# Performance work log

Measured on AMD Instinct MI355X. Metric: run time of the kernel, lower is better.

The kernel has to match this reference:

```python
import jax, jax.numpy as jnp
import numpy as np

MAXU = 6          # init arg maxU
MAXV = 6          # init arg maxV (ratio=None)
TRUNC = 4         # cfg.TRUNCATED_SIZE; cfg.TRUNCATED=True, cfg.FLOW_REG_BY_MAX=True


def setup_inputs() -> dict:
    key = jax.random.key(0)
    B, H, W = 8, 128, 160
    U, V = 2 * MAXU + 1, 2 * MAXV + 1
    x = jax.random.normal(key, (B, 1, U, V, H, W), dtype=jnp.float32)
    return {"x": x}


def reference(x):
    # x: [B,1,U,V,H,W] cost volume
    x = x[:, 0]                                   # [B,U,V,H,W]
    b, u, v, h, w = x.shape

    # --- truncation mask (cfg.TRUNCATED) ---
    # argmax over flattened (u,v); scatter one-hot + MaxPool3d((2t+1,2t+1,1))
    # is equivalent to a +-t box around the per-pixel argmax location.
    idx = jnp.argmax(x.reshape(b, u * v, h, w), axis=1)   # [B,H,W] int
    ui = (idx // v)[:, None, None]                        # [B,1,1,H,W]
    vi = (idx % v)[:, None, None]
    ugrid = jnp.arange(u).reshape(1, u, 1, 1, 1)
    vgrid = jnp.arange(v).reshape(1, 1, v, 1, 1)
    mask = (jnp.abs(ugrid - ui) <= TRUNC) & (jnp.abs(vgrid - vi) <= TRUNC)
    xm = jnp.where(mask, x, -jnp.inf)

    # --- softmax over the U*V displacement hypotheses (FLOW_REG_BY_MAX) ---
    p = jax.nn.softmax(xm.reshape(b, u * v, h, w), axis=1).reshape(b, u, v, h, w)

    dispU = jnp.arange(-MAXU, MAXU + 1, dtype=x.dtype)    # [U]
    dispV = jnp.arange(-MAXV, MAXV + 1, dtype=x.dtype)    # [V]
    flowU = jnp.einsum('buvhw,u->bhw', p, dispU)
    flowV = jnp.einsum('buvhw,v->bhw', p, dispV)
    return jnp.stack((flowU, flowV), axis=1)              # [B,2,H,W]
```

## Files before the change

### kernel.cpp

```cpp
#include <hip/hip_runtime.h>
#include <math.h>

#define Udim 13
#define Vdim 13
#define Hdim 128
#define Wdim 160
#define HW (Hdim * Wdim)
#define UV (Udim * Vdim)
#define TRUNC 4
#define NPIX (8 * HW)
#define NPL 85

__global__ __launch_bounds__(256, 3) void flow_regression_kernel(
    const float* __restrict__ x, float* __restrict__ out) {
    int t    = threadIdx.x;
    int lane = t & 63;
    int g    = lane >> 5;
    int p32  = lane & 31;
    int wave = t >> 6;
    int pixel = blockIdx.x * 128 + wave * 32 + p32;
    int b  = pixel / HW;
    int hw = pixel - b * HW;

    const float* base = x + (size_t)b * UV * HW + hw + (size_t)(g * NPL) * HW;

    float vals[NPL];
    #pragma unroll
    for (int i = 0; i < NPL - 1; ++i) vals[i] = base[(size_t)i * HW];
    vals[NPL - 1] = (g == 0) ? base[(size_t)(NPL - 1) * HW] : -INFINITY;

    float m = vals[0];
    int mi = 0;
    #pragma unroll
    for (int i = 1; i < NPL; ++i)
        if (vals[i] > m) { m = vals[i]; mi = i; }
    mi += g * NPL;

    float om = __shfl_xor(m, 32);
    int   oi = __shfl_xor(mi, 32);
    if (om > m || (om == m && oi < mi)) { m = om; mi = oi; }

    int ui = (mi * 158) >> 11;
    int vi = mi - ui * Vdim;

    float s = 0.f, su = 0.f, sv = 0.f;
    int u = g ? 6 : 0, v = g ? 7 : 0;
    #pragma unroll
    for (int i = 0; i < NPL; ++i) {
        bool in = (u - ui <= TRUNC) && (ui - u <= TRUNC) &&
                  (v - vi <= TRUNC) && (vi - v <= TRUNC);
        float e = in ? __expf(vals[i] - m) : 0.f;
        s  += e;
        su += e * (float)(u - 6);
        sv += e * (float)(v - 6);
        if (++v == Vdim) { v = 0; ++u; }
    }
    s  += __shfl_xor(s, 32);
    su += __shfl_xor(su, 32);
    sv += __shfl_xor(sv, 32);

    if (g == 0) {
        float inv = 1.0f / s;
        float* ob = out + (size_t)b * 2 * HW + hw;
        ob[0]  = su * inv;
        ob[HW] = sv * inv;
    }
}

extern "C" void kernel_launch(void* const* d_in, const int* in_sizes, int n_in,
                              void* d_out, int out_size, void* d_ws, size_t ws_size,
                              hipStream_t stream) {
    const float* x = (const float*)d_in[0];
    float* out = (float*)d_out;
    flow_regression_kernel<<<NPIX / 128, 256, 0, stream>>>(x, out);
}
```

Before: 162.8 us.

## Stage cost volume through LDS with direct global-to-LDS loads, split planes four ways

Each block now stages all 169 planes for 64 pixels into shared memory using global_load_lds, then four lane groups each scan about 43 planes for the argmax and the masked softmax sums. The partial results are combined with shuffles. The goal is to cut per-thread register pressure from the 85-value array and raise occupancy, while keeping loads coalesced. In exchange it uses about 43KB of LDS per block, which limits how many blocks fit per CU, adds a full barrier before any compute, and replaces the constant-multiply divide with a real one.

```diff
diff --git a/kernel.cpp b/kernel.cpp
--- a/kernel.cpp
+++ b/kernel.cpp
@@ -3,65 +3,82 @@
 
 #define Udim 13
 #define Vdim 13
-#define Hdim 128
-#define Wdim 160
-#define HW (Hdim * Wdim)
-#define UV (Udim * Vdim)
+#define HW 20480
+#define UV 169
 #define TRUNC 4
 #define NPIX (8 * HW)
-#define NPL 85
+#define PIX_PER_BLK 64
+#define LDS_STRIDE 65
 
-__global__ __launch_bounds__(256, 3) void flow_regression_kernel(
+typedef const __attribute__((address_space(1))) void glb_void;
+typedef __attribute__((address_space(3))) void lds_void;
+
+__global__ __launch_bounds__(256) void flow_regression_kernel(
     const float* __restrict__ x, float* __restrict__ out) {
+    __shared__ float lds[UV * LDS_STRIDE];
+
     int t    = threadIdx.x;
+    int wave = t >> 6;
     int lane = t & 63;
-    int g    = lane >> 5;
-    int p32  = lane & 31;
-    int wave = t >> 6;
-    int pixel = blockIdx.x * 128 + wave * 32 + p32;
-    int b  = pixel / HW;
-    int hw = pixel - b * HW;
+    int pix0 = blockIdx.x * PIX_PER_BLK;
+    int b    = pix0 / HW;
+    int hw0  = pix0 - b * HW;
 
-    const float* base = x + (size_t)b * UV * HW + hw + (size_t)(g * NPL) * HW;
+    const float* gbase = x + (size_t)b * UV * HW + hw0;
 
-    float vals[NPL];
+    for (int pl = wave; pl < UV; pl += 4) {
+        const float* gp = gbase + (size_t)pl * HW + lane;
+        float* lp = &lds[pl * LDS_STRIDE];
+        __builtin_amdgcn_global_load_lds((glb_void*)gp, (lds_void*)lp, 4, 0, 0);
+    }
+    __builtin_amdgcn_s_waitcnt(0);
+    __syncthreads();
+
+    int q    = lane >> 4;
+    int pcol = (wave << 4) | (lane & 15);
+    int base_pl = q * 43;
+    int npl     = (q == 3) ? 40 : 43;
+
+    float m = -INFINITY;
+    int mi = base_pl;
     #pragma unroll
-    for (int i = 0; i < NPL - 1; ++i) vals[i] = base[(size_t)i * HW];
-    vals[NPL - 1] = (g == 0) ? base[(size_t)(NPL - 1) * HW] : -INFINITY;
-
-    float m = vals[0];
-    int mi = 0;
-    #pragma unroll
-    for (int i = 1; i < NPL; ++i)
-        if (vals[i] > m) { m = vals[i]; mi = i; }
-    mi += g * NPL;
-
-    float om = __shfl_xor(m, 32);
-    int   oi = __shfl_xor(mi, 32);
-    if (om > m || (om == m && oi < mi)) { m = om; mi = oi; }
-
-    int ui = (mi * 158) >> 11;
+    for (int i = 0; i < 43; ++i) {
+        if (i < npl) {
+            float v = lds[(base_pl + i) * LDS_STRIDE + pcol];
+            if (v > m) { m = v; mi = base_pl + i; }
+        }
+    }
+    {
+        float om = __shfl_xor(m, 16); int oi = __shfl_xor(mi, 16);
+        if (om > m || (om == m && oi < mi)) { m = om; mi = oi; }
+        om = __shfl_xor(m, 32); oi = __shfl_xor(mi, 32);
+        if (om > m || (om == m && oi < mi)) { m = om; mi = oi; }
+    }
+    int ui = mi / Vdim;
     int vi = mi - ui * Vdim;
 
     float s = 0.f, su = 0.f, sv = 0.f;
-    int u = g ? 6 : 0, v = g ? 7 : 0;
+    int u = base_pl / Vdim;
+    int v = base_pl - u * Vdim;
     #pragma unroll
-    for (int i = 0; i < NPL; ++i) {
-        bool in = (u - ui <= TRUNC) && (ui - u <= TRUNC) &&
-                  (v - vi <= TRUNC) && (vi - v <= TRUNC);
-        float e = in ? __expf(vals[i] - m) : 0.f;
-        s  += e;
-        su += e * (float)(u - 6);
-        sv += e * (float)(v - 6);
+    for (int i = 0; i < 43; ++i) {
+        if (i < npl) {
+            float val = lds[(base_pl + i) * LDS_STRIDE + pcol];
+            bool in = (u - ui <= TRUNC) && (ui - u <= TRUNC) &&
+                      (v - vi <= TRUNC) && (vi - v <= TRUNC);
+            float e = in ? __expf(val - m) : 0.f;
+            s  += e;
+            su += e * (float)(u - 6);
+            sv += e * (float)(v - 6);
+        }
         if (++v == Vdim) { v = 0; ++u; }
     }
-    s  += __shfl_xor(s, 32);
-    su += __shfl_xor(su, 32);
-    sv += __shfl_xor(sv, 32);
+    s  += __shfl_xor(s, 16);  su += __shfl_xor(su, 16);  sv += __shfl_xor(sv, 16);
+    s  += __shfl_xor(s, 32);  su += __shfl_xor(su, 32);  sv += __shfl_xor(sv, 32);
 
-    if (g == 0) {
+    if (q == 0) {
         float inv = 1.0f / s;
-        float* ob = out + (size_t)b * 2 * HW + hw;
+        float* ob = out + (size_t)b * 2 * HW + (hw0 + pcol);
         ob[0]  = su * inv;
         ob[HW] = sv * inv;
     }
@@ -72,5 +89,5 @@
                               hipStream_t stream) {
     const float* x = (const float*)d_in[0];
     float* out = (float*)d_out;
-    flow_regression_kernel<<<NPIX / 128, 256, 0, stream>>>(x, out);
+    flow_regression_kernel<<<NPIX / PIX_PER_BLK, 256, 0, stream>>>(x, out);
 }
```

New measurement: 163.1 us. Within noise of the previous version (+0.2%).

## Split each pixel's displacement planes across four lane groups instead of two

Applied to the files above, without the earlier changes.

Each pixel's 169 cost planes are now spread over four 16-lane groups of 43 planes each, instead of two 32-lane groups of 85. This cuts per-thread register arrays and raises occupancy (launch bounds 3→4), giving more loads in flight for this bandwidth-bound kernel. The cost is an extra shuffle stage for both the argmax and sum reductions. Each wave also reads only 16 contiguous pixels per plane, which gives shorter coalesced segments, and the grid doubles.

```diff
diff --git a/kernel.cpp b/kernel.cpp
--- a/kernel.cpp
+++ b/kernel.cpp
@@ -1,50 +1,58 @@
 #include <hip/hip_runtime.h>
 #include <math.h>
 
-#define Udim 13
 #define Vdim 13
-#define Hdim 128
-#define Wdim 160
-#define HW (Hdim * Wdim)
-#define UV (Udim * Vdim)
+#define HW 20480
+#define UV 169
 #define TRUNC 4
 #define NPIX (8 * HW)
-#define NPL 85
+#define PPB 64
+#define NPL 43
 
-__global__ __launch_bounds__(256, 3) void flow_regression_kernel(
+__global__ __launch_bounds__(256, 4) void flow_regression_kernel(
     const float* __restrict__ x, float* __restrict__ out) {
     int t    = threadIdx.x;
+    int wave = t >> 6;
     int lane = t & 63;
-    int g    = lane >> 5;
-    int p32  = lane & 31;
-    int wave = t >> 6;
-    int pixel = blockIdx.x * 128 + wave * 32 + p32;
-    int b  = pixel / HW;
-    int hw = pixel - b * HW;
+    int q    = lane >> 4;
+    int pcol = (wave << 4) | (lane & 15);
+    int pix0 = blockIdx.x * PPB;
+    int b    = pix0 / HW;
+    int hw   = pix0 - b * HW + pcol;
+    int base_pl = q * NPL;
 
-    const float* base = x + (size_t)b * UV * HW + hw + (size_t)(g * NPL) * HW;
+    const float* gp = x + (size_t)b * UV * HW + hw;
 
     float vals[NPL];
     #pragma unroll
-    for (int i = 0; i < NPL - 1; ++i) vals[i] = base[(size_t)i * HW];
-    vals[NPL - 1] = (g == 0) ? base[(size_t)(NPL - 1) * HW] : -INFINITY;
+    for (int i = 0; i < 40; ++i)
+        vals[i] = gp[(size_t)(base_pl + i) * HW];
+    #pragma unroll
+    for (int i = 40; i < NPL; ++i) {
+        int pl   = base_pl + i;
+        bool pad = pl >= UV;
+        float v  = gp[(size_t)(pad ? (UV - 1) : pl) * HW];
+        vals[i]  = pad ? -INFINITY : v;
+    }
+    #pragma unroll
+    for (int i = 0; i < NPL; ++i) asm volatile("" : "+v"(vals[i]));
 
     float m = vals[0];
-    int mi = 0;
+    int  mi = base_pl;
     #pragma unroll
     for (int i = 1; i < NPL; ++i)
-        if (vals[i] > m) { m = vals[i]; mi = i; }
-    mi += g * NPL;
-
-    float om = __shfl_xor(m, 32);
-    int   oi = __shfl_xor(mi, 32);
-    if (om > m || (om == m && oi < mi)) { m = om; mi = oi; }
-
+        if (vals[i] > m) { m = vals[i]; mi = base_pl + i; }
+    {
+        float om = __shfl_xor(m, 16); int oi = __shfl_xor(mi, 16);
+        if (om > m || (om == m && oi < mi)) { m = om; mi = oi; }
+        om = __shfl_xor(m, 32); oi = __shfl_xor(mi, 32);
+        if (om > m || (om == m && oi < mi)) { m = om; mi = oi; }
+    }
     int ui = (mi * 158) >> 11;
     int vi = mi - ui * Vdim;
 
     float s = 0.f, su = 0.f, sv = 0.f;
-    int u = g ? 6 : 0, v = g ? 7 : 0;
+    int u = 3 * q, v = 4 * q;
     #pragma unroll
     for (int i = 0; i < NPL; ++i) {
         bool in = (u - ui <= TRUNC) && (ui - u <= TRUNC) &&
@@ -55,11 +63,10 @@
         sv += e * (float)(v - 6);
         if (++v == Vdim) { v = 0; ++u; }
     }
-    s  += __shfl_xor(s, 32);
-    su += __shfl_xor(su, 32);
-    sv += __shfl_xor(sv, 32);
+    s  += __shfl_xor(s, 16);  su += __shfl_xor(su, 16);  sv += __shfl_xor(sv, 16);
+    s  += __shfl_xor(s, 32);  su += __shfl_xor(su, 32);  sv += __shfl_xor(sv, 32);
 
-    if (g == 0) {
+    if (q == 0) {
         float inv = 1.0f / s;
         float* ob = out + (size_t)b * 2 * HW + hw;
         ob[0]  = su * inv;
@@ -72,5 +79,5 @@
                               hipStream_t stream) {
     const float* x = (const float*)d_in[0];
     float* out = (float*)d_out;
-    flow_regression_kernel<<<NPIX / 128, 256, 0, stream>>>(x, out);
+    flow_regression_kernel<<<NPIX / PPB, 256, 0, stream>>>(x, out);
 }
```

Result: no change. 165.7 us (+1.8%).
